# Optimization experiments

Hardware: AMD Instinct MI355X
Metric: run time of the kernel (lower is better)

Reference implementation:

```python
import jax, jax.numpy as jnp
import numpy as np

KH = KW = 3
SH = SW = 1
PAD = 1
IN_LEN = 8
OUT_LEN = 16
NUM_ITERS = 3


def squash(t, axis=-1):
    sq = jnp.sum(t * t, axis=axis, keepdims=True)
    return (sq / (1.0 + sq)) * t / jnp.sqrt(sq)


def setup_inputs() -> dict:
    key = jax.random.key(0)
    k1, k2 = jax.random.split(key)
    x = jax.random.normal(k1, (4, 64, 32, 32), dtype=jnp.float32)
    # weight: (out_channels//out_length, C_in//in_length * kh*kw, out_length, in_length)
    weight = jax.random.normal(k2, (8, 72, 16, 8), dtype=jnp.float32)
    return {"x": x, "weight": weight}


def reference(x, weight):
    N, C, H, W = x.shape
    O = weight.shape[0]
    L = OUT_LEN
    G = C // IN_LEN  # number of input capsule groups
    Ho = 1 + (H + 2 * PAD - KH) // SH
    Wo = 1 + (W + 2 * PAD - KW) // SW

    # im2col: (N, C*KH*KW, Ho, Wo), feature dim ordered channel-major, kernel-spatial-minor
    patches = jax.lax.conv_general_dilated_patches(
        x, (KH, KW), (SH, SW), [(PAD, PAD), (PAD, PAD)])
    # -> (N, G, in_length, kk, Ho*Wo)
    pt = patches.reshape(N, G, IN_LEN, KH * KW, Ho * Wo)
    # -> (N, HW, G, kk, in_length), matching torch's unfold/view/transpose chain
    pt = jnp.transpose(pt, (0, 4, 1, 3, 2))
    win = pt.reshape(N, Ho * Wo, G * KH * KW, IN_LEN)

    priors = jnp.einsum('oflp,nwfp->nowfl', weight, win)
    priors = priors.reshape(N, O, Ho * Wo, G, KH * KW, L)

    # dynamic routing
    probs = jnp.ones(priors.shape[:-1] + (1,), priors.dtype)
    outputs = None
    for r in range(NUM_ITERS):
        s = jnp.mean(jnp.sum(probs * priors, axis=-2, keepdims=True),
                     axis=-3, keepdims=True)  # (N,O,HW,1,1,L)
        outputs = squash(s)
        if r != NUM_ITERS - 1:
            delta = jnp.sum(priors * outputs, axis=-1, keepdims=True)
            probs = probs + jnp.exp(delta)

    out = outputs[:, :, :, 0, 0, :]                    # (N, O, HW, L)
    out = jnp.transpose(out, (0, 1, 3, 2))             # (N, O, L, HW)
    return out.reshape(N, O * L, Ho, Wo)
```

## Files before the change

### kernel.cpp

```cpp
#include <hip/hip_runtime.h>
#include <hip/hip_bf16.h>


typedef short bf16x8 __attribute__((ext_vector_type(8)));
typedef float f32x4 __attribute__((ext_vector_type(4)));
typedef unsigned int uint2v __attribute__((ext_vector_type(2)));

__device__ __forceinline__ float red16(float v) {
#if __has_builtin(__builtin_amdgcn_permlane16_swap)
  uint2v r = __builtin_amdgcn_permlane16_swap(__float_as_uint(v), __float_as_uint(v),
                                              false, false);
  return __uint_as_float(r[0]) + __uint_as_float(r[1]);
#else
  return v + __shfl_xor(v, 16);
#endif
}

__device__ __forceinline__ float red32(float v) {
#if __has_builtin(__builtin_amdgcn_permlane32_swap)
  uint2v r = __builtin_amdgcn_permlane32_swap(__float_as_uint(v), __float_as_uint(v),
                                              false, false);
  return __uint_as_float(r[0]) + __uint_as_float(r[1]);
#else
  return v + __shfl_xor(v, 32);
#endif
}

__device__ __forceinline__ uint pack_split(float v) {
  __hip_bfloat16 hb = __float2bfloat16(v);
  float hf = __bfloat162float(hb);
  __hip_bfloat16 lb = __float2bfloat16(v - hf);
  return (uint)(*(ushort*)&hb) | ((uint)(*(ushort*)&lb) << 16);
}

__global__ __launch_bounds__(256)
void prep(const float* __restrict__ x, const float* __restrict__ w,
          ushort* __restrict__ wT, ushort* __restrict__ xT) {
  const int b = blockIdx.x;
  if (b < 128) {
    __shared__ uint lds[32 * 65];
    const int n = b >> 5, h0 = b & 31;
    const float* src = x + n * 65536 + h0 * 32;
    for (int i = threadIdx.x; i < 2048; i += 256) {
      const int c = i >> 5, p = i & 31;
      lds[p * 65 + c] = pack_split(src[c * 1024 + p]);
    }
    __syncthreads();
    uint* dst = (uint*)xT + (n * 1024 + h0 * 32) * 64;
    for (int i = threadIdx.x; i < 512; i += 256) {
      const int pix = i >> 4, seg = i & 15;
      const uint* row = &lds[pix * 65 + (seg & 7) * 8];
      uint4 v;
      if (seg < 8) {
        v.x = (row[0] & 0xffffu) | (row[1] << 16);
        v.y = (row[2] & 0xffffu) | (row[3] << 16);
        v.z = (row[4] & 0xffffu) | (row[5] << 16);
        v.w = (row[6] & 0xffffu) | (row[7] << 16);
      } else {
        v.x = (row[0] >> 16) | (row[1] & 0xffff0000u);
        v.y = (row[2] >> 16) | (row[3] & 0xffff0000u);
        v.z = (row[4] >> 16) | (row[5] & 0xffff0000u);
        v.w = (row[6] >> 16) | (row[7] & 0xffff0000u);
      }
      *(uint4*)(dst + pix * 64 + seg * 4) = v;
    }
  } else {
    const int t = (b - 128) * 256 + threadIdx.x;
    if (t >= 9216) return;
    const float* src = w + t * 8;
    uint hi[4], lo[4];
    #pragma unroll
    for (int p2 = 0; p2 < 4; ++p2) {
      uint a = pack_split(src[p2 * 2]);
      uint c = pack_split(src[p2 * 2 + 1]);
      hi[p2] = (a & 0xffffu) | (c << 16);
      lo[p2] = (a >> 16) | (c & 0xffff0000u);
    }
    uint* dstp = (uint*)(wT + t * 16);
    *(uint4*)dstp       = make_uint4(hi[0], hi[1], hi[2], hi[3]);
    *(uint4*)(dstp + 4) = make_uint4(lo[0], lo[1], lo[2], lo[3]);
  }
}

__global__ __launch_bounds__(256, 3)
void caps_main(const ushort* __restrict__ wT, const ushort* __restrict__ xT,
               float* __restrict__ out) {
  const int b  = blockIdx.x;
  const int wt = b & 1, h = (b >> 1) & 31, o = (b >> 6) & 7, n = b >> 9;
  const int w0 = wt * 16;
  const int tid = threadIdx.x, lane = tid & 63, fq = tid >> 6;
  const int pix = lane & 15, q = lane >> 4;

  __shared__ uint  xs[54 * 68];
  __shared__ float sbuf[2][4 * 256];

  for (int i = tid; i < 54 * 16; i += 256) {
    const int r = i >> 4, seg = i & 15;
    const int kh = r / 18, c = r % 18;
    const int hh = h + kh - 1, ww = w0 + c - 1;
    uint4 v = make_uint4(0u, 0u, 0u, 0u);
    if ((unsigned)hh < 32u && (unsigned)ww < 32u) {
      const uint* g = (const uint*)xT + (n * 1024 + hh * 32 + ww) * 64 + seg * 4;
      v = *(const uint4*)g;
    }
    *(uint4*)&xs[r * 68 + seg * 4] = v;
  }
  __syncthreads();

  f32x4 P[18];
  const f32x4 zacc = {0.f, 0.f, 0.f, 0.f};
  const ushort* wA = wT + ((o * 72 + fq * 18) * 16 + pix) * 16 + ((q >= 2) ? 8 : 0);
  const int xw_lane = pix * 68 + ((q & 1) ? 32 : 0);
  #pragma unroll
  for (int j = 0; j < 18; ++j) {
    const int g = fq * 2 + (j >= 9 ? 1 : 0);
    const int s = j % 9, kh = s / 3, kw = s % 3;
    const bf16x8 a  = *(const bf16x8*)(wA + j * 256);
    const bf16x8 bv = *(const bf16x8*)&xs[(kh * 18 + kw) * 68 + g * 4 + xw_lane];
    P[j] = __builtin_amdgcn_mfma_f32_16x16x32_bf16(a, bv, zacc, 0, 0, 0);
  }

  float c[18];
  #pragma unroll
  for (int j = 0; j < 18; ++j) c[j] = 1.f;

  const int sidx = pix * 16 + (((q + (pix >> 1)) & 3) << 2);
  #pragma unroll
  for (int it = 0; it < 3; ++it) {
    f32x4 sp = {0.f, 0.f, 0.f, 0.f};
    #pragma unroll
    for (int j = 0; j < 18; ++j) {
      sp.x += c[j] * P[j].x; sp.y += c[j] * P[j].y;
      sp.z += c[j] * P[j].z; sp.w += c[j] * P[j].w;
    }
    float* sb = sbuf[it & 1];
    *(f32x4*)&sb[fq * 256 + sidx] = sp;
    __syncthreads();
    f32x4 sv = *(const f32x4*)&sb[sidx];
    #pragma unroll
    for (int k4 = 1; k4 < 4; ++k4) {
      f32x4 t = *(const f32x4*)&sb[k4 * 256 + sidx];
      sv.x += t.x; sv.y += t.y; sv.z += t.z; sv.w += t.w;
    }
    sv.x *= 0.125f; sv.y *= 0.125f; sv.z *= 0.125f; sv.w *= 0.125f;
    float qq = sv.x * sv.x + sv.y * sv.y + sv.z * sv.z + sv.w * sv.w;
    qq = red32(red16(qq));
    const float k = sqrtf(qq) / (1.f + qq);
    f32x4 ov;
    ov.x = sv.x * k; ov.y = sv.y * k; ov.z = sv.z * k; ov.w = sv.w * k;
    if (it < 2) {
      #pragma unroll
      for (int j = 0; j < 18; ++j) {
        float d = P[j].x * ov.x + P[j].y * ov.y + P[j].z * ov.z + P[j].w * ov.w;
        d = red32(red16(d));
        c[j] += __expf(d);
      }
    } else if (fq == 0) {
      float* op = out + ((n * 8 + o) * 16 + (q << 2)) * 1024 + h * 32 + w0 + pix;
      op[0]    = ov.x;
      op[1024] = ov.y;
      op[2048] = ov.z;
      op[3072] = ov.w;
    }
  }
}

extern "C" void kernel_launch(void* const* d_in, const int* in_sizes, int n_in,
                              void* d_out, int out_size, void* d_ws, size_t ws_size,
                              hipStream_t stream) {
  const float* x = (const float*)d_in[0];
  const float* w = (const float*)d_in[1];
  float* outp    = (float*)d_out;
  ushort* wT = (ushort*)d_ws;
  ushort* xT = (ushort*)((char*)d_ws + 294912);
  prep<<<dim3(164), dim3(256), 0, stream>>>(x, w, wT, xT);
  caps_main<<<dim3(2048), dim3(256), 0, stream>>>(wT, xT, outp);
}
```

Measured before the change: 75.67 us.

## Fuse input bf16 split-packing into main kernel tile load

Removes the x transpose/split stage from the prep kernel and instead has each main block load raw fp32 input directly, split it into hi/lo bf16 and scatter into the LDS tile in the channel-minor layout. This drops one global round trip of the packed input and shrinks the prep launch to weights only. It also raises the occupancy hint to 4 blocks per SM. In exchange each block does redundant conversion work and uses strided scalar global loads and 2-byte LDS stores instead of 16-byte vector copies.

```diff
diff --git a/kernel.cpp b/kernel.cpp
--- a/kernel.cpp
+++ b/kernel.cpp
@@ -34,56 +34,25 @@
 }
 
 __global__ __launch_bounds__(256)
-void prep(const float* __restrict__ x, const float* __restrict__ w,
-          ushort* __restrict__ wT, ushort* __restrict__ xT) {
-  const int b = blockIdx.x;
-  if (b < 128) {
-    __shared__ uint lds[32 * 65];
-    const int n = b >> 5, h0 = b & 31;
-    const float* src = x + n * 65536 + h0 * 32;
-    for (int i = threadIdx.x; i < 2048; i += 256) {
-      const int c = i >> 5, p = i & 31;
-      lds[p * 65 + c] = pack_split(src[c * 1024 + p]);
-    }
-    __syncthreads();
-    uint* dst = (uint*)xT + (n * 1024 + h0 * 32) * 64;
-    for (int i = threadIdx.x; i < 512; i += 256) {
-      const int pix = i >> 4, seg = i & 15;
-      const uint* row = &lds[pix * 65 + (seg & 7) * 8];
-      uint4 v;
-      if (seg < 8) {
-        v.x = (row[0] & 0xffffu) | (row[1] << 16);
-        v.y = (row[2] & 0xffffu) | (row[3] << 16);
-        v.z = (row[4] & 0xffffu) | (row[5] << 16);
-        v.w = (row[6] & 0xffffu) | (row[7] << 16);
-      } else {
-        v.x = (row[0] >> 16) | (row[1] & 0xffff0000u);
-        v.y = (row[2] >> 16) | (row[3] & 0xffff0000u);
-        v.z = (row[4] >> 16) | (row[5] & 0xffff0000u);
-        v.w = (row[6] >> 16) | (row[7] & 0xffff0000u);
-      }
-      *(uint4*)(dst + pix * 64 + seg * 4) = v;
-    }
-  } else {
-    const int t = (b - 128) * 256 + threadIdx.x;
-    if (t >= 9216) return;
-    const float* src = w + t * 8;
-    uint hi[4], lo[4];
-    #pragma unroll
-    for (int p2 = 0; p2 < 4; ++p2) {
-      uint a = pack_split(src[p2 * 2]);
-      uint c = pack_split(src[p2 * 2 + 1]);
-      hi[p2] = (a & 0xffffu) | (c << 16);
-      lo[p2] = (a >> 16) | (c & 0xffff0000u);
-    }
-    uint* dstp = (uint*)(wT + t * 16);
-    *(uint4*)dstp       = make_uint4(hi[0], hi[1], hi[2], hi[3]);
-    *(uint4*)(dstp + 4) = make_uint4(lo[0], lo[1], lo[2], lo[3]);
+void prep(const float* __restrict__ w, ushort* __restrict__ wT) {
+  const int t = blockIdx.x * 256 + threadIdx.x;
+  if (t >= 9216) return;
+  const float* src = w + t * 8;
+  uint hi[4], lo[4];
+  #pragma unroll
+  for (int p2 = 0; p2 < 4; ++p2) {
+    uint a = pack_split(src[p2 * 2]);
+    uint c = pack_split(src[p2 * 2 + 1]);
+    hi[p2] = (a & 0xffffu) | (c << 16);
+    lo[p2] = (a >> 16) | (c & 0xffff0000u);
   }
+  uint* dstp = (uint*)(wT + t * 16);
+  *(uint4*)dstp       = make_uint4(hi[0], hi[1], hi[2], hi[3]);
+  *(uint4*)(dstp + 4) = make_uint4(lo[0], lo[1], lo[2], lo[3]);
 }
 
-__global__ __launch_bounds__(256, 3)
-void caps_main(const ushort* __restrict__ wT, const ushort* __restrict__ xT,
+__global__ __launch_bounds__(256, 4)
+void caps_main(const ushort* __restrict__ wT, const float* __restrict__ xsrc,
                float* __restrict__ out) {
   const int b  = blockIdx.x;
   const int wt = b & 1, h = (b >> 1) & 31, o = (b >> 6) & 7, n = b >> 9;
@@ -93,17 +62,18 @@
 
   __shared__ uint  xs[54 * 68];
   __shared__ float sbuf[2][4 * 256];
+  ushort* usx = (ushort*)xs;
 
-  for (int i = tid; i < 54 * 16; i += 256) {
-    const int r = i >> 4, seg = i & 15;
-    const int kh = r / 18, c = r % 18;
-    const int hh = h + kh - 1, ww = w0 + c - 1;
-    uint4 v = make_uint4(0u, 0u, 0u, 0u);
-    if ((unsigned)hh < 32u && (unsigned)ww < 32u) {
-      const uint* g = (const uint*)xT + (n * 1024 + hh * 32 + ww) * 64 + seg * 4;
-      v = *(const uint4*)g;
-    }
-    *(uint4*)&xs[r * 68 + seg * 4] = v;
+  for (int i = tid; i < 3456; i += 256) {
+    const int c = i / 54, r = i - c * 54;
+    const int kh = r / 18, col = r - kh * 18;
+    const int hh = h + kh - 1, ww = w0 + col - 1;
+    float v = 0.f;
+    if ((unsigned)hh < 32u && (unsigned)ww < 32u)
+      v = xsrc[((n * 64 + c) * 32 + hh) * 32 + ww];
+    const uint pk = pack_split(v);
+    usx[r * 136 + c]      = (ushort)(pk & 0xffffu);
+    usx[r * 136 + 64 + c] = (ushort)(pk >> 16);
   }
   __syncthreads();
 
@@ -172,7 +142,6 @@
   const float* w = (const float*)d_in[1];
   float* outp    = (float*)d_out;
   ushort* wT = (ushort*)d_ws;
-  ushort* xT = (ushort*)((char*)d_ws + 294912);
-  prep<<<dim3(164), dim3(256), 0, stream>>>(x, w, wT, xT);
-  caps_main<<<dim3(2048), dim3(256), 0, stream>>>(wT, xT, outp);
+  prep<<<dim3(36), dim3(256), 0, stream>>>(w, wT);
+  caps_main<<<dim3(2048), dim3(256), 0, stream>>>(wT, x, outp);
 }
```

New measurement: 82.17 us. +8.6%, slower.
